# Performance work log

Hardware: AMD Instinct MI355X
Metric: run time of the kernel (lower is better)

The kernel has to match this reference:

```python
import jax, jax.numpy as jnp
import numpy as np

B, Ng, A, Eg = 32, 2500, 50, 2000      # graphs, atoms/graph, residues/graph, edges/graph
DIN, EDIM, H1, H2, AF, HG = 64, 16, 64, 64, 95, 128
F1, F2, F3 = 64, 32, 16
K, T = 3, 6                             # ARMA num_stacks, num_layers
N, E = B * Ng, B * Eg


def _glorot(k, shape, fan_in):
    return jax.random.normal(k, shape, jnp.float32) / np.sqrt(fan_in)


def setup_inputs():
    key = jax.random.key(0)
    ks = jax.random.split(key, 24)
    x = jax.random.normal(ks[0], (N, DIN), jnp.float32)
    off = (jnp.arange(B) * Ng)[:, None]
    src = (jax.random.randint(ks[1], (B, Eg), 0, Ng) + off).reshape(-1)
    dst = (jax.random.randint(ks[2], (B, Eg), 0, Ng) + off).reshape(-1)
    edge_index = jnp.stack([src, dst])
    edge_attr = jax.random.normal(ks[3], (E, EDIM), jnp.float32)
    monomer_labels = jnp.tile(jnp.arange(Ng) // (Ng // A), B)  # atom -> residue (0..A-1, per graph)
    aminoacids_features = jax.random.normal(ks[4], (B, A, AF), jnp.float32)
    FIN = H2 + AF  # 159, ARMA input dim
    return {
        'x': x, 'edge_index': edge_index, 'edge_attr': edge_attr,
        'monomer_labels': monomer_labels, 'aminoacids_features': aminoacids_features,
        'w_e1': _glorot(ks[5], (EDIM, DIN * H1), EDIM), 'b_e1': jnp.zeros((DIN * H1,)),
        'root1': _glorot(ks[6], (DIN, H1), DIN), 'bias1': jnp.zeros((H1,)),
        'w_e2': _glorot(ks[7], (EDIM, H1 * H2), EDIM), 'b_e2': jnp.zeros((H1 * H2,)),
        'root2': _glorot(ks[8], (H1, H2), H1), 'bias2': jnp.zeros((H2,)),
        'attn_atom_w': _glorot(ks[9], (H2, 1), H2), 'attn_atom_b': jnp.zeros((1,)),
        'arma_init_w': _glorot(ks[10], (K, FIN, HG), FIN),
        'arma_w': _glorot(ks[11], (T - 1, K, HG, HG), HG),
        'arma_root_w': _glorot(ks[12], (T, K, FIN, HG), FIN),
        'arma_bias': jnp.zeros((T, K, 1, HG)),
        'attn_aa_w': _glorot(ks[13], (HG, 1), HG), 'attn_aa_b': jnp.zeros((1,)),
        'w1': _glorot(ks[14], (HG, F1), HG), 'b1': jnp.zeros((F1,)),
        'w2': _glorot(ks[15], (F1, F2), F1), 'b2': jnp.zeros((F2,)),
        'w3': _glorot(ks[16], (F2, F3), F2), 'b3': jnp.zeros((F3,)),
        'w4': _glorot(ks[17], (F3, 1), F3), 'b4': jnp.zeros((1,)),
    }


def reference(x, edge_index, edge_attr, monomer_labels, aminoacids_features,
              w_e1, b_e1, root1, bias1, w_e2, b_e2, root2, bias2,
              attn_atom_w, attn_atom_b, arma_init_w, arma_w, arma_root_w, arma_bias,
              attn_aa_w, attn_aa_b, w1, b1, w2, b2, w3, b3, w4, b4):
    src, dst = edge_index[0], edge_index[1]

    def nnconv(h, w_e, b_e, root, bias):
        din, dout = root.shape
        W = (edge_attr @ w_e + b_e).reshape(-1, din, dout)      # per-edge weight [E, din, dout]
        msg = jnp.einsum('ei,eio->eo', h[src], W)               # per-edge matvec
        agg = jax.ops.segment_sum(msg, dst, num_segments=N)     # scatter-add at dst
        return agg + h @ root + bias

    h = jax.nn.relu(nnconv(x, w_e1, b_e1, root1, bias1))
    h = jax.nn.relu(nnconv(h, w_e2, b_e2, root2, bias2))

    # AttentionReadoutAtom per graph: softmax over atoms, scatter-sum to residues
    hb = h.reshape(B, Ng, H2)
    attn = jax.nn.softmax(hb @ attn_atom_w + attn_atom_b, axis=1)
    wx = (hb * attn).reshape(-1, H2)
    seg = (monomer_labels.reshape(B, Ng) + jnp.arange(B)[:, None] * A).reshape(-1)
    amino = jax.ops.segment_sum(wx, seg, num_segments=B * A).reshape(B, A, H2)
    xi = jnp.concatenate([amino, aminoacids_features], axis=-1)  # [B, A, H2+95]

    # ARMAConv over directed residue chain i->i+1; gcn_norm w/o self-loops:
    # node 0 has in-degree 0 so edge (0,1) gets norm 0, all others norm 1.
    norm = jnp.concatenate([jnp.zeros(1), jnp.ones(A - 2)])      # [A-1]

    def prop(z):  # z: [B, K, A, F]; out[i+1] = norm_i * z[i]
        shifted = z[..., :-1, :] * norm[:, None]
        return jnp.concatenate([jnp.zeros_like(z[..., :1, :]), shifted], axis=-2)

    out = prop(jnp.einsum('baf,kfg->bkag', xi, arma_init_w))
    out = jax.nn.relu(out + jnp.einsum('baf,kfg->bkag', xi, arma_root_w[0]) + arma_bias[0][None])
    for t in range(1, T):
        out = prop(jnp.einsum('bkaf,kfg->bkag', out, arma_w[t - 1]))
        out = jax.nn.relu(out + jnp.einsum('baf,kfg->bkag', xi, arma_root_w[t]) + arma_bias[t][None])
    g = jax.nn.relu(out.mean(axis=1))  # mean over K stacks -> [B, A, HG]

    # AttentionReadoutAminoAcid: softmax over residues, weighted sum
    a = jax.nn.softmax(g @ attn_aa_w + attn_aa_b, axis=1)
    p = (g * a).sum(axis=1)  # [B, HG]

    # MLP head (dropout is identity in eval mode)
    p = jax.nn.relu(p @ w1 + b1)
    p = jax.nn.relu(p @ w2 + b2)
    p = jax.nn.relu(p @ w3 + b3)
    return (p @ w4 + b4).reshape(-1)
```

## Files before the change

kernel.cpp:

```cpp
#include <hip/hip_runtime.h>

#define N_NODES 80000
#define N_EDGES 64000
#define NB      32
#define NG      2500
#define NA      50
#define EDIM    16
#define FIN     159
#define HG      128
#define RICOLS  2688

typedef __attribute__((ext_vector_type(8))) short bf16x8;
typedef __attribute__((ext_vector_type(4))) float f32x4;

__device__ inline ushort rne_bf16(float f) {
    union { float f; unsigned u; } v; v.f = f;
    const unsigned r = v.u + 0x7fffu + ((v.u >> 16) & 1u);
    return (ushort)(r >> 16);
}
__device__ inline float bf16_to_f32(ushort h) {
    union { unsigned u; float f; } v; v.u = ((unsigned)h) << 16;
    return v.f;
}
__device__ __forceinline__ void gl_lds16(const void* gsrc, void* ldst) {
    __builtin_amdgcn_global_load_lds(
        (const __attribute__((address_space(1))) unsigned int*)gsrc,
        (__attribute__((address_space(3))) unsigned int*)ldst, 16, 0, 0);
}

__global__ __launch_bounds__(256) void prep_w2(const float* __restrict__ we1, const float* __restrict__ be1,
    const float* __restrict__ we2, const float* __restrict__ be2,
    ushort* __restrict__ w1h, ushort* __restrict__ w1l, ushort* __restrict__ w2h, ushort* __restrict__ w2l)
{
    int idx = blockIdx.x * 256 + threadIdx.x;
    const int half = (idx >= 17 * 8 * 64) ? 1 : 0;
    if (half) idx -= 17 * 8 * 64;
    if (idx >= 17 * 8 * 64) return;
    const float* we = half ? we2 : we1;
    const float* be = half ? be2 : be1;
    ushort* Wh = half ? w2h : w1h;
    ushort* Wlo = half ? w2l : w1l;
    const int l = idx & 63;
    const int slot = (idx >> 6) & 7;
    const int j = idx >> 9;
    const int n = slot >> 1, kq = slot & 1;
    const int o = n * 16 + (l & 15);
    const int i0 = kq * 32 + (l >> 4) * 8;
    ushort th[8], tl[8];
#pragma unroll
    for (int t = 0; t < 8; ++t) {
        const int i = i0 + t;
        const float f = (j < 16) ? we[j * 4096 + i * 64 + o] : be[i * 64 + o];
        const ushort hi = rne_bf16(f);
        th[t] = hi;
        tl[t] = rne_bf16(f - bf16_to_f32(hi));
    }
    *(uint4*)(Wh + (size_t)idx * 8) = *(const uint4*)th;
    *(uint4*)(Wlo + (size_t)idx * 8) = *(const uint4*)tl;
}

template<int RELU>
__global__ __launch_bounds__(256) void root_gemm(const float* __restrict__ in,
    const float* __restrict__ w, const float* __restrict__ bias, float* __restrict__ out)
{
    __shared__ float At[64 * 65];
    __shared__ float Wl[64 * 64];
    __shared__ float bl[64];
    const int tid = threadIdx.x;
    const int r0 = blockIdx.x * 64;
    for (int s = tid; s < 4096; s += 256) {
        int r = s >> 6, c = s & 63;
        float v = in[(r0 + r) * 64 + c];
        if (RELU) v = fmaxf(v, 0.f);
        At[c * 65 + r] = v;
    }
    for (int s = tid; s < 4096; s += 256) Wl[s] = w[s];
    if (tid < 64) bl[tid] = bias[tid];
    __syncthreads();
    const int tr = tid >> 4, tc = tid & 15;
    float acc[4][4] = {};
#pragma unroll 8
    for (int i = 0; i < 64; ++i) {
        const float4 a4 = *(const float4*)&At[i * 65 + tr * 4];
        const float4 b4 = *(const float4*)&Wl[i * 64 + tc * 4];
        const float av[4] = {a4.x, a4.y, a4.z, a4.w};
        const float bv[4] = {b4.x, b4.y, b4.z, b4.w};
#pragma unroll
        for (int m = 0; m < 4; ++m)
#pragma unroll
            for (int n = 0; n < 4; ++n) acc[m][n] = fmaf(av[m], bv[n], acc[m][n]);
    }
    const float4 bq = *(const float4*)&bl[tc * 4];
#pragma unroll
    for (int m = 0; m < 4; ++m) {
        float4 o4 = {acc[m][0] + bq.x, acc[m][1] + bq.y, acc[m][2] + bq.z, acc[m][3] + bq.w};
        *(float4*)&out[(r0 + tr * 4 + m) * 64 + tc * 4] = o4;
    }
}

#define TE 128
template<int RELU>
__global__ __launch_bounds__(256) void edge_conv_mfma(const float* __restrict__ h,
    const float* __restrict__ ea, const int* __restrict__ src, const int* __restrict__ dst,
    const ushort* __restrict__ Whi, const ushort* __restrict__ Wlo, float* __restrict__ agg)
{
    __shared__ ushort Bst[2][8192];
    __shared__ float  EAt[17 * 132];
    const int tid = threadIdx.x;
    const int e0 = blockIdx.x * TE;
    const int wv = tid >> 6, l = tid & 63;

#pragma unroll
    for (int i = 0; i < 4; ++i) {
        const int c = wv * 4 + i;
        const ushort* gs = (c < 8) ? (Whi + ((size_t)c * 64 + l) * 8)
                                   : (Wlo + ((size_t)(c - 8) * 64 + l) * 8);
        gl_lds16(gs, (char*)(&Bst[0][0]) + c * 1024);
    }
    for (int s = tid; s < TE * 16; s += 256) {
        const int le = s >> 4, j = s & 15;
        EAt[j * 132 + le] = ea[(size_t)(e0 + le) * 16 + j];
    }
    if (tid < TE) EAt[16 * 132 + tid] = 1.0f;

    bf16x8 ah[2][2], al[2][2];
#pragma unroll
    for (int m = 0; m < 2; ++m) {
        const int erow = wv * 32 + m * 16 + (l & 15);
        const int nd = src[e0 + erow];
        const float4* hp = (const float4*)(h + (size_t)nd * 64);
#pragma unroll
        for (int kq = 0; kq < 2; ++kq) {
            const int q0 = kq * 8 + (l >> 4) * 2;
            const float4 v0 = hp[q0], v1 = hp[q0 + 1];
            const float fv[8] = {v0.x, v0.y, v0.z, v0.w, v1.x, v1.y, v1.z, v1.w};
            ushort th[8], tl[8];
#pragma unroll
            for (int t = 0; t < 8; ++t) {
                const float f = RELU ? fmaxf(fv[t], 0.f) : fv[t];
                th[t] = rne_bf16(f);
                tl[t] = rne_bf16(f - bf16_to_f32(th[t]));
            }
            ah[m][kq] = *(const bf16x8*)th;
            al[m][kq] = *(const bf16x8*)tl;
        }
    }
    __syncthreads();

    f32x4 msg[2][4];
#pragma unroll
    for (int m = 0; m < 2; ++m)
#pragma unroll
        for (int n = 0; n < 4; ++n) msg[m][n] = (f32x4)0.f;

#pragma unroll 1
    for (int j = 0; j < 17; ++j) {
        const int cur = j & 1;
        if (j < 16) {
#pragma unroll
            for (int i = 0; i < 4; ++i) {
                const int c = wv * 4 + i;
                const ushort* gs = (c < 8) ? (Whi + ((size_t)((j + 1) * 8 + c) * 64 + l) * 8)
                                           : (Wlo + ((size_t)((j + 1) * 8 + (c - 8)) * 64 + l) * 8);
                gl_lds16(gs, (char*)(&Bst[cur ^ 1][0]) + c * 1024);
            }
        }
        f32x4 eam[2];
        eam[0] = *(const f32x4*)&EAt[j * 132 + wv * 32 + (l >> 4) * 4];
        eam[1] = *(const f32x4*)&EAt[j * 132 + wv * 32 + 16 + (l >> 4) * 4];
#pragma unroll
        for (int n = 0; n < 4; ++n) {
            const char* bb = (const char*)(&Bst[cur][0]);
            const bf16x8 bh0 = *(const bf16x8*)(bb + ((n * 2 + 0) * 64 + l) * 16);
            const bf16x8 bh1 = *(const bf16x8*)(bb + ((n * 2 + 1) * 64 + l) * 16);
            const bf16x8 bl0 = *(const bf16x8*)(bb + 8192 + ((n * 2 + 0) * 64 + l) * 16);
            const bf16x8 bl1 = *(const bf16x8*)(bb + 8192 + ((n * 2 + 1) * 64 + l) * 16);
#pragma unroll
            for (int m = 0; m < 2; ++m) {
                f32x4 t = __builtin_amdgcn_mfma_f32_16x16x32_bf16(ah[m][0], bh0, (f32x4)0.f, 0, 0, 0);
                t = __builtin_amdgcn_mfma_f32_16x16x32_bf16(ah[m][1], bh1, t, 0, 0, 0);
                t = __builtin_amdgcn_mfma_f32_16x16x32_bf16(ah[m][0], bl0, t, 0, 0, 0);
                t = __builtin_amdgcn_mfma_f32_16x16x32_bf16(ah[m][1], bl1, t, 0, 0, 0);
                t = __builtin_amdgcn_mfma_f32_16x16x32_bf16(al[m][0], bh0, t, 0, 0, 0);
                t = __builtin_amdgcn_mfma_f32_16x16x32_bf16(al[m][1], bh1, t, 0, 0, 0);
                msg[m][n] += eam[m] * t;
            }
        }
        __syncthreads();
    }

#pragma unroll
    for (int m = 0; m < 2; ++m)
#pragma unroll
        for (int r = 0; r < 4; ++r) {
            const int erow = wv * 32 + m * 16 + (l >> 4) * 4 + r;
            const size_t d = (size_t)dst[e0 + erow] * 64;
#pragma unroll
            for (int n = 0; n < 4; ++n)
                atomicAdd(&agg[d + n * 16 + (l & 15)], msg[m][n][r]);
        }
}

__global__ __launch_bounds__(256) void pool_k(const float* __restrict__ h2,
    const float* __restrict__ waw, const float* __restrict__ wab,
    const float* __restrict__ aaf, float* __restrict__ xi)
{
    __shared__ float wl[64];
    __shared__ float sc[NG];
    __shared__ float red[256];
    const int g = blockIdx.x, tid = threadIdx.x;
    if (tid < 64) wl[tid] = waw[tid];
    __syncthreads();
    const size_t gb = (size_t)g * NG;
    const float bia = wab[0];
    for (int a = tid; a < NG; a += 256) {
        const float4* hp = (const float4*)(h2 + (gb + a) * 64);
        float acc = bia;
#pragma unroll
        for (int q = 0; q < 16; ++q) {
            const float4 v = hp[q];
            acc = fmaf(fmaxf(v.x, 0.f), wl[q * 4 + 0], acc);
            acc = fmaf(fmaxf(v.y, 0.f), wl[q * 4 + 1], acc);
            acc = fmaf(fmaxf(v.z, 0.f), wl[q * 4 + 2], acc);
            acc = fmaf(fmaxf(v.w, 0.f), wl[q * 4 + 3], acc);
        }
        sc[a] = acc;
    }
    __syncthreads();
    float m = -1e30f;
    for (int a = tid; a < NG; a += 256) m = fmaxf(m, sc[a]);
    red[tid] = m; __syncthreads();
    for (int st = 128; st; st >>= 1) { if (tid < st) red[tid] = fmaxf(red[tid], red[tid + st]); __syncthreads(); }
    const float mx = red[0]; __syncthreads();
    float s = 0.f;
    for (int a = tid; a < NG; a += 256) { const float e = expf(sc[a] - mx); sc[a] = e; s += e; }
    red[tid] = s; __syncthreads();
    for (int st = 128; st; st >>= 1) { if (tid < st) red[tid] += red[tid + st]; __syncthreads(); }
    const float inv = 1.0f / red[0];
    __syncthreads();
    for (int idx = tid; idx < NA * 64; idx += 256) {
        const int res = idx >> 6, o = idx & 63;
        const size_t rb = gb + (size_t)res * 50;
        float acc = 0.f;
#pragma unroll 10
        for (int i = 0; i < 50; ++i)
            acc = fmaf(sc[res * 50 + i], fmaxf(h2[(rb + i) * 64 + o], 0.f), acc);
        xi[((size_t)g * NA + res) * FIN + o] = acc * inv;
    }
    for (int s2 = tid; s2 < NA * 95; s2 += 256) {
        const int lr = s2 / 95, f = s2 % 95;
        xi[((size_t)g * NA + lr) * FIN + 64 + f] = aaf[((size_t)g * NA + lr) * 95 + f];
    }
}

__global__ __launch_bounds__(256) void ri_gemm(const float* __restrict__ xi,
    const float* __restrict__ rootw, const float* __restrict__ initw,
    const float* __restrict__ abias, float* __restrict__ RI)
{
    __shared__ float At[32 * 65];
    __shared__ float Bl[32 * 64];
    const int tid = threadIdx.x;
    const int r0 = blockIdx.x * 64, c0 = blockIdx.y * 64;
    const int blk = c0 >> 7;
    const int gb = c0 & 127;
    const float* bsrc = (blk < 18) ? (rootw + (long)blk * FIN * 128) : (initw + (long)(blk - 18) * FIN * 128);
    const int tr = tid >> 4, tc = tid & 15;
    float acc[4][4] = {};
    for (int f0 = 0; f0 < FIN; f0 += 32) {
        __syncthreads();
        for (int s = tid; s < 64 * 32; s += 256) {
            const int r = s >> 5, kk = s & 31; const int f = f0 + kk;
            At[kk * 65 + r] = (f < FIN) ? xi[(long)(r0 + r) * FIN + f] : 0.f;
        }
        for (int s = tid; s < 32 * 64; s += 256) {
            const int kk = s >> 6, cc = s & 63; const int f = f0 + kk;
            Bl[s] = (f < FIN) ? bsrc[(long)f * 128 + gb + cc] : 0.f;
        }
        __syncthreads();
#pragma unroll 8
        for (int kk = 0; kk < 32; ++kk) {
            const float4 a4 = *(const float4*)&At[kk * 65 + tr * 4];
            const float4 b4 = *(const float4*)&Bl[kk * 64 + tc * 4];
            const float av[4] = {a4.x, a4.y, a4.z, a4.w};
            const float bv[4] = {b4.x, b4.y, b4.z, b4.w};
#pragma unroll
            for (int m = 0; m < 4; ++m)
#pragma unroll
                for (int n = 0; n < 4; ++n) acc[m][n] = fmaf(av[m], bv[n], acc[m][n]);
        }
    }
    float4 bq = {0.f, 0.f, 0.f, 0.f};
    if (blk < 18) bq = *(const float4*)&abias[c0 + tc * 4];
#pragma unroll
    for (int m = 0; m < 4; ++m) {
        float4 o4 = {acc[m][0] + bq.x, acc[m][1] + bq.y, acc[m][2] + bq.z, acc[m][3] + bq.w};
        *(float4*)&RI[(long)(r0 + tr * 4 + m) * RICOLS + c0 + tc * 4] = o4;
    }
}

__global__ __launch_bounds__(512) void arma_all(const float* __restrict__ RI,
    const float* __restrict__ armaw, float* __restrict__ G)
{
    __shared__ float X0[NA * 128];
    __shared__ float X1[NA * 128];
    __shared__ float Wl[128 * 128];
    const int bid = blockIdx.x;
    const int g = bid / 3, k = bid % 3;
    const int tid = threadIdx.x;
    const size_t rbase = (size_t)g * NA;

    for (int s = tid; s < NA * 128; s += 512) {
        const int a = s >> 7, o = s & 127;
        float v = RI[(rbase + a) * RICOLS + k * 128 + o];
        if (a >= 2) v += RI[(rbase + a - 1) * RICOLS + (18 + k) * 128 + o];
        X0[s] = fmaxf(v, 0.f);
    }
    float* cur = X0;
    float* nxt = X1;
    const int q = tid & 31;
    const int rh = tid >> 5;
    for (int t = 1; t <= 5; ++t) {
        __syncthreads();
        const float* W = armaw + (size_t)((t - 1) * 3 + k) * 16384;
        for (int s = tid; s < 4096; s += 512) ((float4*)Wl)[s] = ((const float4*)W)[s];
        __syncthreads();
        for (int a = rh; a < NA; a += 16) {
            float4 acc = {0.f, 0.f, 0.f, 0.f};
            if (a >= 2) {
                const float* xr = cur + (a - 1) * 128;
#pragma unroll 8
                for (int f0 = 0; f0 < 128; f0 += 4) {
                    const float4 xv = *(const float4*)(xr + f0);
                    const float4 w0 = *(const float4*)&Wl[(f0 + 0) * 128 + q * 4];
                    const float4 w1 = *(const float4*)&Wl[(f0 + 1) * 128 + q * 4];
                    const float4 w2 = *(const float4*)&Wl[(f0 + 2) * 128 + q * 4];
                    const float4 w3 = *(const float4*)&Wl[(f0 + 3) * 128 + q * 4];
                    acc.x = fmaf(xv.x, w0.x, acc.x); acc.y = fmaf(xv.x, w0.y, acc.y);
                    acc.z = fmaf(xv.x, w0.z, acc.z); acc.w = fmaf(xv.x, w0.w, acc.w);
                    acc.x = fmaf(xv.y, w1.x, acc.x); acc.y = fmaf(xv.y, w1.y, acc.y);
                    acc.z = fmaf(xv.y, w1.z, acc.z); acc.w = fmaf(xv.y, w1.w, acc.w);
                    acc.x = fmaf(xv.z, w2.x, acc.x); acc.y = fmaf(xv.z, w2.y, acc.y);
                    acc.z = fmaf(xv.z, w2.z, acc.z); acc.w = fmaf(xv.z, w2.w, acc.w);
                    acc.x = fmaf(xv.w, w3.x, acc.x); acc.y = fmaf(xv.w, w3.y, acc.y);
                    acc.z = fmaf(xv.w, w3.z, acc.z); acc.w = fmaf(xv.w, w3.w, acc.w);
                }
            }
            const float4 rv = *(const float4*)&RI[(rbase + a) * RICOLS + (t * 3 + k) * 128 + q * 4];
            float4 ov = {fmaxf(acc.x + rv.x, 0.f), fmaxf(acc.y + rv.y, 0.f),
                         fmaxf(acc.z + rv.z, 0.f), fmaxf(acc.w + rv.w, 0.f)};
            *(float4*)(nxt + a * 128 + q * 4) = ov;
        }
        float* tmp = cur; cur = nxt; nxt = tmp;
    }
    __syncthreads();
    for (int s = tid; s < NA * 128; s += 512)
        atomicAdd(&G[rbase * 128 + s], cur[s] * (1.f / 3.f));
}

__global__ __launch_bounds__(256) void final_k(const float* __restrict__ G,
    const float* __restrict__ waa, const float* __restrict__ baa,
    const float* __restrict__ w1, const float* __restrict__ b1,
    const float* __restrict__ w2, const float* __restrict__ b2,
    const float* __restrict__ w3, const float* __restrict__ b3,
    const float* __restrict__ w4, const float* __restrict__ b4, float* __restrict__ out)
{
    __shared__ float gl[50 * 129];
    __shared__ float sc[64];
    __shared__ float pl[128];
    __shared__ float h1l[64], h2l[32], h3l[16];
    __shared__ float wl[128];
    const int b = blockIdx.x, tid = threadIdx.x;
    for (int s = tid; s < 50 * 128; s += 256) {
        const int a = s >> 7, o = s & 127;
        gl[a * 129 + o] = fmaxf(G[((size_t)b * 50 + a) * 128 + o], 0.f);
    }
    if (tid < 128) wl[tid] = waa[tid];
    __syncthreads();
    if (tid < 50) {
        float acc = baa[0];
        for (int f = 0; f < 128; ++f) acc = fmaf(gl[tid * 129 + f], wl[f], acc);
        sc[tid] = acc;
    }
    __syncthreads();
    if (tid < 64) {
        const float v = (tid < 50) ? sc[tid] : -1e30f;
        float m = v;
        for (int d = 32; d; d >>= 1) m = fmaxf(m, __shfl_xor(m, d));
        const float e = (tid < 50) ? expf(v - m) : 0.f;
        float ssum = e;
        for (int d = 32; d; d >>= 1) ssum += __shfl_xor(ssum, d);
        if (tid < 50) sc[tid] = e / ssum;
    }
    __syncthreads();
    if (tid < 128) {
        float acc = 0.f;
        for (int a = 0; a < 50; ++a) acc = fmaf(sc[a], gl[a * 129 + tid], acc);
        pl[tid] = acc;
    }
    __syncthreads();
    if (tid < 64) {
        float acc = b1[tid];
        for (int f = 0; f < 128; ++f) acc = fmaf(pl[f], w1[f * 64 + tid], acc);
        h1l[tid] = fmaxf(acc, 0.f);
    }
    __syncthreads();
    if (tid < 32) {
        float acc = b2[tid];
        for (int f = 0; f < 64; ++f) acc = fmaf(h1l[f], w2[f * 32 + tid], acc);
        h2l[tid] = fmaxf(acc, 0.f);
    }
    __syncthreads();
    if (tid < 16) {
        float acc = b3[tid];
        for (int f = 0; f < 32; ++f) acc = fmaf(h2l[f], w3[f * 16 + tid], acc);
        h3l[tid] = fmaxf(acc, 0.f);
    }
    __syncthreads();
    if (tid == 0) {
        float acc = b4[0];
        for (int f = 0; f < 16; ++f) acc = fmaf(h3l[f], w4[f], acc);
        out[b] = acc;
    }
}

extern "C" void kernel_launch(void* const* d_in, const int* in_sizes, int n_in,
                              void* d_out, int out_size, void* d_ws, size_t ws_size,
                              hipStream_t stream) {
    const float* x     = (const float*)d_in[0];
    const int*   eidx  = (const int*)d_in[1];
    const float* ea    = (const float*)d_in[2];
    const float* aaf   = (const float*)d_in[4];
    const float* we1   = (const float*)d_in[5];
    const float* be1   = (const float*)d_in[6];
    const float* root1 = (const float*)d_in[7];
    const float* bias1 = (const float*)d_in[8];
    const float* we2   = (const float*)d_in[9];
    const float* be2   = (const float*)d_in[10];
    const float* root2 = (const float*)d_in[11];
    const float* bias2 = (const float*)d_in[12];
    const float* waw   = (const float*)d_in[13];
    const float* wab   = (const float*)d_in[14];
    const float* initw = (const float*)d_in[15];
    const float* armaw = (const float*)d_in[16];
    const float* rootw = (const float*)d_in[17];
    const float* abias = (const float*)d_in[18];
    const float* waa   = (const float*)d_in[19];
    const float* baa   = (const float*)d_in[20];
    const float* w1    = (const float*)d_in[21];
    const float* b1    = (const float*)d_in[22];
    const float* w2    = (const float*)d_in[23];
    const float* b2    = (const float*)d_in[24];
    const float* w3    = (const float*)d_in[25];
    const float* b3    = (const float*)d_in[26];
    const float* w4    = (const float*)d_in[27];
    const float* b4    = (const float*)d_in[28];
    float* out = (float*)d_out;

    const int* src = eidx;
    const int* dst = eidx + N_EDGES;

    char* ws = (char*)d_ws;
    size_t off = 0;
    float* h1     = (float*)(ws + off); off += (size_t)N_NODES * 64 * 4;
    float* h2     = (float*)(ws + off); off += (size_t)N_NODES * 64 * 4;
    float* xi     = (float*)(ws + off); off += (size_t)1600 * FIN * 4;
    float* RI     = (float*)(ws + off); off += (size_t)1600 * RICOLS * 4;
    float* G      = (float*)(ws + off); off += (size_t)1600 * 128 * 4;
    ushort* wt1h  = (ushort*)(ws + off); off += (size_t)17 * 8 * 64 * 8 * 2;
    ushort* wt1l  = (ushort*)(ws + off); off += (size_t)17 * 8 * 64 * 8 * 2;
    ushort* wt2h  = (ushort*)(ws + off); off += (size_t)17 * 8 * 64 * 8 * 2;
    ushort* wt2l  = (ushort*)(ws + off); off += (size_t)17 * 8 * 64 * 8 * 2;

    prep_w2<<<68, 256, 0, stream>>>(we1, be1, we2, be2, wt1h, wt1l, wt2h, wt2l);

    root_gemm<0><<<N_NODES / 64, 256, 0, stream>>>(x, root1, bias1, h1);
    edge_conv_mfma<0><<<N_EDGES / TE, 256, 0, stream>>>(x, ea, src, dst, wt1h, wt1l, h1);
    root_gemm<1><<<N_NODES / 64, 256, 0, stream>>>(h1, root2, bias2, h2);
    edge_conv_mfma<1><<<N_EDGES / TE, 256, 0, stream>>>(h1, ea, src, dst, wt2h, wt2l, h2);
    pool_k<<<NB, 256, 0, stream>>>(h2, waw, wab, aaf, xi);
    ri_gemm<<<dim3(25, 42), 256, 0, stream>>>(xi, rootw, initw, abias, RI);
    hipMemsetAsync(G, 0, (size_t)1600 * 128 * 4, stream);
    arma_all<<<NB * 3, 512, 0, stream>>>(RI, armaw, G);
    final_k<<<NB, 256, 0, stream>>>(G, waa, baa, w1, b1, w2, b2, w3, b3, w4, b4, out);
}
```

Baseline: 373.2 us.

## Split atom pooling into parallel kernels and halve ARMA blocks with register tiling

Replaces the 32-block pooling kernel with three kernels: a grid-wide per-atom score pass, a per-graph softmax, and a per-residue weighted-sum kernel with 400 blocks. The ARMA kernel now splits each graph/stack into two overlapping row halves (recomputing a halo), uses a 4x4 register tile, and writes per-stack outputs instead of atomics, removing the memset. The final kernel averages the three stack buffers. This adds launches and redundant halo compute in exchange for far more parallelism in the low-occupancy tail stages.

After: 347.9 us. 1.07x faster.

```diff
diff --git a/kernel.cpp b/kernel.cpp
--- a/kernel.cpp
+++ b/kernel.cpp
@@ -201,55 +201,60 @@
         }
 }
 
-__global__ __launch_bounds__(256) void pool_k(const float* __restrict__ h2,
-    const float* __restrict__ waw, const float* __restrict__ wab,
-    const float* __restrict__ aaf, float* __restrict__ xi)
+__global__ __launch_bounds__(256) void scores_k(const float* __restrict__ h2,
+    const float* __restrict__ w, const float* __restrict__ b, float* __restrict__ sc)
 {
     __shared__ float wl[64];
-    __shared__ float sc[NG];
+    if (threadIdx.x < 64) wl[threadIdx.x] = w[threadIdx.x];
+    __syncthreads();
+    const int n = blockIdx.x * 256 + threadIdx.x;
+    if (n < N_NODES) {
+        float acc = b[0];
+        const float4* hp = (const float4*)(h2 + (long)n * 64);
+#pragma unroll
+        for (int q = 0; q < 16; ++q) {
+            const float4 v = hp[q];
+            acc = fmaf(fmaxf(v.x, 0.f), wl[q * 4 + 0], acc); acc = fmaf(fmaxf(v.y, 0.f), wl[q * 4 + 1], acc);
+            acc = fmaf(fmaxf(v.z, 0.f), wl[q * 4 + 2], acc); acc = fmaf(fmaxf(v.w, 0.f), wl[q * 4 + 3], acc);
+        }
+        sc[n] = acc;
+    }
+}
+
+__global__ __launch_bounds__(256) void softmax_k(const float* __restrict__ sc, float* __restrict__ attn)
+{
     __shared__ float red[256];
     const int g = blockIdx.x, tid = threadIdx.x;
-    if (tid < 64) wl[tid] = waw[tid];
-    __syncthreads();
-    const size_t gb = (size_t)g * NG;
-    const float bia = wab[0];
-    for (int a = tid; a < NG; a += 256) {
-        const float4* hp = (const float4*)(h2 + (gb + a) * 64);
-        float acc = bia;
-#pragma unroll
-        for (int q = 0; q < 16; ++q) {
-            const float4 v = hp[q];
-            acc = fmaf(fmaxf(v.x, 0.f), wl[q * 4 + 0], acc);
-            acc = fmaf(fmaxf(v.y, 0.f), wl[q * 4 + 1], acc);
-            acc = fmaf(fmaxf(v.z, 0.f), wl[q * 4 + 2], acc);
-            acc = fmaf(fmaxf(v.w, 0.f), wl[q * 4 + 3], acc);
-        }
-        sc[a] = acc;
-    }
-    __syncthreads();
+    const float* s = sc + (long)g * NG;
     float m = -1e30f;
-    for (int a = tid; a < NG; a += 256) m = fmaxf(m, sc[a]);
+    for (int a = tid; a < NG; a += 256) m = fmaxf(m, s[a]);
     red[tid] = m; __syncthreads();
     for (int st = 128; st; st >>= 1) { if (tid < st) red[tid] = fmaxf(red[tid], red[tid + st]); __syncthreads(); }
     const float mx = red[0]; __syncthreads();
-    float s = 0.f;
-    for (int a = tid; a < NG; a += 256) { const float e = expf(sc[a] - mx); sc[a] = e; s += e; }
-    red[tid] = s; __syncthreads();
+    float sum = 0.f;
+    for (int a = tid; a < NG; a += 256) sum += expf(s[a] - mx);
+    red[tid] = sum; __syncthreads();
     for (int st = 128; st; st >>= 1) { if (tid < st) red[tid] += red[tid + st]; __syncthreads(); }
     const float inv = 1.0f / red[0];
-    __syncthreads();
-    for (int idx = tid; idx < NA * 64; idx += 256) {
-        const int res = idx >> 6, o = idx & 63;
-        const size_t rb = gb + (size_t)res * 50;
-        float acc = 0.f;
+    for (int a = tid; a < NG; a += 256) attn[(long)g * NG + a] = expf(s[a] - mx) * inv;
+}
+
+__global__ __launch_bounds__(256) void amino_k(const float* __restrict__ h2,
+    const float* __restrict__ attn, const float* __restrict__ aa, float* __restrict__ xi)
+{
+    const int tid = threadIdx.x;
+    const int r = blockIdx.x * 4 + (tid >> 6);
+    const int o = tid & 63;
+    const int g = r / NA, ar = r % NA;
+    const long base = (long)g * NG + ar * 50;
+    float acc = 0.f;
 #pragma unroll 10
-        for (int i = 0; i < 50; ++i)
-            acc = fmaf(sc[res * 50 + i], fmaxf(h2[(rb + i) * 64 + o], 0.f), acc);
-        xi[((size_t)g * NA + res) * FIN + o] = acc * inv;
-    }
-    for (int s2 = tid; s2 < NA * 95; s2 += 256) {
-        const int lr = s2 / 95, f = s2 % 95;
-        xi[((size_t)g * NA + lr) * FIN + 64 + f] = aaf[((size_t)g * NA + lr) * 95 + f];
+    for (int a = 0; a < 50; ++a) acc = fmaf(attn[base + a], fmaxf(h2[(base + a) * 64 + o], 0.f), acc);
+    xi[(long)r * FIN + o] = acc;
+    for (int s = tid; s < 4 * 95; s += 256) {
+        const int lr = s / 95, f = s % 95;
+        const int rr = blockIdx.x * 4 + lr;
+        xi[(long)rr * FIN + 64 + f] = aa[(long)rr * 95 + f];
     }
 }
 
@@ -298,63 +303,75 @@
     }
 }
 
-__global__ __launch_bounds__(512) void arma_all(const float* __restrict__ RI,
+__global__ __launch_bounds__(256) void arma_all(const float* __restrict__ RI,
     const float* __restrict__ armaw, float* __restrict__ G)
 {
-    __shared__ float X0[NA * 128];
-    __shared__ float X1[NA * 128];
+    __shared__ float X[2][32 * 128];
     __shared__ float Wl[128 * 128];
     const int bid = blockIdx.x;
-    const int g = bid / 3, k = bid % 3;
+    const int g = bid / 6, k = (bid % 6) >> 1, half = bid & 1;
     const int tid = threadIdx.x;
+    const int r0 = half ? 20 : 0;
     const size_t rbase = (size_t)g * NA;
 
-    for (int s = tid; s < NA * 128; s += 512) {
-        const int a = s >> 7, o = s & 127;
+    for (int s = tid; s < 30 * 128; s += 256) {
+        const int a = r0 + (s >> 7), o = s & 127;
         float v = RI[(rbase + a) * RICOLS + k * 128 + o];
         if (a >= 2) v += RI[(rbase + a - 1) * RICOLS + (18 + k) * 128 + o];
-        X0[s] = fmaxf(v, 0.f);
-    }
-    float* cur = X0;
-    float* nxt = X1;
-    const int q = tid & 31;
-    const int rh = tid >> 5;
+        X[0][s] = fmaxf(v, 0.f);
+    }
+    int cur = 0;
+    const int rg = tid >> 5;
+    const int cg = tid & 31;
     for (int t = 1; t <= 5; ++t) {
         __syncthreads();
         const float* W = armaw + (size_t)((t - 1) * 3 + k) * 16384;
-        for (int s = tid; s < 4096; s += 512) ((float4*)Wl)[s] = ((const float4*)W)[s];
+        for (int s = tid; s < 4096; s += 256) ((float4*)Wl)[s] = ((const float4*)W)[s];
         __syncthreads();
-        for (int a = rh; a < NA; a += 16) {
-            float4 acc = {0.f, 0.f, 0.f, 0.f};
-            if (a >= 2) {
-                const float* xr = cur + (a - 1) * 128;
-#pragma unroll 8
-                for (int f0 = 0; f0 < 128; f0 += 4) {
-                    const float4 xv = *(const float4*)(xr + f0);
-                    const float4 w0 = *(const float4*)&Wl[(f0 + 0) * 128 + q * 4];
-                    const float4 w1 = *(const float4*)&Wl[(f0 + 1) * 128 + q * 4];
-                    const float4 w2 = *(const float4*)&Wl[(f0 + 2) * 128 + q * 4];
-                    const float4 w3 = *(const float4*)&Wl[(f0 + 3) * 128 + q * 4];
-                    acc.x = fmaf(xv.x, w0.x, acc.x); acc.y = fmaf(xv.x, w0.y, acc.y);
-                    acc.z = fmaf(xv.x, w0.z, acc.z); acc.w = fmaf(xv.x, w0.w, acc.w);
-                    acc.x = fmaf(xv.y, w1.x, acc.x); acc.y = fmaf(xv.y, w1.y, acc.y);
-                    acc.z = fmaf(xv.y, w1.z, acc.z); acc.w = fmaf(xv.y, w1.w, acc.w);
-                    acc.x = fmaf(xv.z, w2.x, acc.x); acc.y = fmaf(xv.z, w2.y, acc.y);
-                    acc.z = fmaf(xv.z, w2.z, acc.z); acc.w = fmaf(xv.z, w2.w, acc.w);
-                    acc.x = fmaf(xv.w, w3.x, acc.x); acc.y = fmaf(xv.w, w3.y, acc.y);
-                    acc.z = fmaf(xv.w, w3.z, acc.z); acc.w = fmaf(xv.w, w3.w, acc.w);
+        float acc[4][4] = {};
+#pragma unroll 4
+        for (int f0 = 0; f0 < 128; f0 += 4) {
+            float4 wv[4];
+#pragma unroll
+            for (int i = 0; i < 4; ++i) wv[i] = *(const float4*)&Wl[(f0 + i) * 128 + cg * 4];
+#pragma unroll
+            for (int m = 0; m < 4; ++m) {
+                const int lr = rg * 4 + m;
+                const int pl = (lr >= 1) ? lr - 1 : 0;
+                const float4 xv = *(const float4*)&X[cur][pl * 128 + f0];
+#pragma unroll
+                for (int n = 0; n < 4; ++n) {
+                    acc[m][n] = fmaf(xv.x, ((const float*)&wv[0])[n], acc[m][n]);
+                    acc[m][n] = fmaf(xv.y, ((const float*)&wv[1])[n], acc[m][n]);
+                    acc[m][n] = fmaf(xv.z, ((const float*)&wv[2])[n], acc[m][n]);
+                    acc[m][n] = fmaf(xv.w, ((const float*)&wv[3])[n], acc[m][n]);
                 }
             }
-            const float4 rv = *(const float4*)&RI[(rbase + a) * RICOLS + (t * 3 + k) * 128 + q * 4];
-            float4 ov = {fmaxf(acc.x + rv.x, 0.f), fmaxf(acc.y + rv.y, 0.f),
-                         fmaxf(acc.z + rv.z, 0.f), fmaxf(acc.w + rv.w, 0.f)};
-            *(float4*)(nxt + a * 128 + q * 4) = ov;
-        }
-        float* tmp = cur; cur = nxt; nxt = tmp;
-    }
-    __syncthreads();
-    for (int s = tid; s < NA * 128; s += 512)
-        atomicAdd(&G[rbase * 128 + s], cur[s] * (1.f / 3.f));
+        }
+        __syncthreads();
+#pragma unroll
+        for (int m = 0; m < 4; ++m) {
+            const int lr = rg * 4 + m;
+            if (lr < 30) {
+                const int a = r0 + lr;
+                const bool prop = (a >= 2) && (lr >= 1);
+                const float4 rv = *(const float4*)&RI[(rbase + a) * RICOLS + (t * 3 + k) * 128 + cg * 4];
+                float4 ov;
+                ov.x = fmaxf((prop ? acc[m][0] : 0.f) + rv.x, 0.f);
+                ov.y = fmaxf((prop ? acc[m][1] : 0.f) + rv.y, 0.f);
+                ov.z = fmaxf((prop ? acc[m][2] : 0.f) + rv.z, 0.f);
+                ov.w = fmaxf((prop ? acc[m][3] : 0.f) + rv.w, 0.f);
+                *(float4*)&X[cur ^ 1][lr * 128 + cg * 4] = ov;
+            }
+        }
+        cur ^= 1;
+    }
+    __syncthreads();
+    const int w0 = half ? 25 : 0;
+    for (int s = tid; s < 25 * 128; s += 256) {
+        const int a = w0 + (s >> 7), o = s & 127;
+        G[((size_t)k * 1600 + rbase + a) * 128 + o] = X[cur][(a - r0) * 128 + o];
+    }
 }
 
 __global__ __launch_bounds__(256) void final_k(const float* __restrict__ G,
@@ -372,7 +389,9 @@
     const int b = blockIdx.x, tid = threadIdx.x;
     for (int s = tid; s < 50 * 128; s += 256) {
         const int a = s >> 7, o = s & 127;
-        gl[a * 129 + o] = fmaxf(G[((size_t)b * 50 + a) * 128 + o], 0.f);
+        const size_t r = ((size_t)b * 50 + a) * 128 + o;
+        const float v = (G[r] + G[(size_t)1600 * 128 + r] + G[(size_t)2 * 1600 * 128 + r]) * (1.f / 3.f);
+        gl[a * 129 + o] = fmaxf(v, 0.f);
     }
     if (tid < 128) wl[tid] = waa[tid];
     __syncthreads();
@@ -463,9 +482,11 @@
     size_t off = 0;
     float* h1     = (float*)(ws + off); off += (size_t)N_NODES * 64 * 4;
     float* h2     = (float*)(ws + off); off += (size_t)N_NODES * 64 * 4;
+    float* scores = (float*)(ws + off); off += (size_t)N_NODES * 4;
+    float* attn   = (float*)(ws + off); off += (size_t)N_NODES * 4;
     float* xi     = (float*)(ws + off); off += (size_t)1600 * FIN * 4;
     float* RI     = (float*)(ws + off); off += (size_t)1600 * RICOLS * 4;
-    float* G      = (float*)(ws + off); off += (size_t)1600 * 128 * 4;
+    float* G      = (float*)(ws + off); off += (size_t)3 * 1600 * 128 * 4;
     ushort* wt1h  = (ushort*)(ws + off); off += (size_t)17 * 8 * 64 * 8 * 2;
     ushort* wt1l  = (ushort*)(ws + off); off += (size_t)17 * 8 * 64 * 8 * 2;
     ushort* wt2h  = (ushort*)(ws + off); off += (size_t)17 * 8 * 64 * 8 * 2;
@@ -477,9 +498,10 @@
     edge_conv_mfma<0><<<N_EDGES / TE, 256, 0, stream>>>(x, ea, src, dst, wt1h, wt1l, h1);
     root_gemm<1><<<N_NODES / 64, 256, 0, stream>>>(h1, root2, bias2, h2);
     edge_conv_mfma<1><<<N_EDGES / TE, 256, 0, stream>>>(h1, ea, src, dst, wt2h, wt2l, h2);
-    pool_k<<<NB, 256, 0, stream>>>(h2, waw, wab, aaf, xi);
+    scores_k<<<(N_NODES + 255) / 256, 256, 0, stream>>>(h2, waw, wab, scores);
+    softmax_k<<<NB, 256, 0, stream>>>(scores, attn);
+    amino_k<<<1600 / 4, 256, 0, stream>>>(h2, attn, aaf, xi);
     ri_gemm<<<dim3(25, 42), 256, 0, stream>>>(xi, rootw, initw, abias, RI);
-    hipMemsetAsync(G, 0, (size_t)1600 * 128 * 4, stream);
-    arma_all<<<NB * 3, 512, 0, stream>>>(RI, armaw, G);
+    arma_all<<<NB * 6, 256, 0, stream>>>(RI, armaw, G);
     final_k<<<NB, 256, 0, stream>>>(G, waa, baa, w1, b1, w2, b2, w3, b3, w4, b4, out);
 }
```
